# Kernel tuning notes

Measured on AMD Instinct MI355X. Metric: run time of the kernel, lower is better.

The kernel has to match this reference:

```python
import jax, jax.numpy as jnp
import numpy as np

B, T, D, H = 8, 4096, 128, 64


def setup_inputs() -> dict:
    key = jax.random.key(0)
    kx, kf, kg = jax.random.split(key, 3)
    X = jax.random.normal(kx, (B, T, D), dtype=jnp.float32)
    Wf = jax.random.normal(kf, (D, H), dtype=jnp.float32) * 0.05   # Conv1D k=1 weight
    Wg = jax.random.normal(kg, (3, D, H), dtype=jnp.float32) * 0.05  # Conv1D k=3 weight
    return {"X": X, "Wf": Wf, "Wg": Wg}


def reference(X, Wf, Wg):
    # f(X): pointwise conv == matmul over feature dim
    f = jnp.einsum('btd,dh->bth', X, Wf)
    # g(X): kernel-3 'same' conv, taps at offsets -1,0,+1
    Xp = jnp.pad(X, ((0, 0), (1, 1), (0, 0)))
    Tlen = X.shape[1]
    g = (jnp.einsum('btd,dh->bth', Xp[:, 0:Tlen], Wg[0])
         + jnp.einsum('btd,dh->bth', Xp[:, 1:Tlen + 1], Wg[1])
         + jnp.einsum('btd,dh->bth', Xp[:, 2:Tlen + 2], Wg[2]))
    # scores [B,T,T], scaled by sqrt(h)
    M = jnp.einsum('bth,bsh->bts', f, g) / jnp.sqrt(jnp.float32(H))
    w = jax.nn.softmax(M, axis=-1)
    # values are the raw input X
    return jnp.einsum('bts,bsd->btd', w, X)
```

## Files before the change

### kernel.cpp

```cpp
#include <hip/hip_runtime.h>
#include <hip/hip_bf16.h>

#define B_ 8
#define T_ 4096
#define D_ 128
#define H_ 64
#define SBLK 64
#define NT (T_ / SBLK)
#define NT2 (NT / 2)

typedef short bf16x8 __attribute__((ext_vector_type(8)));
typedef float f32x4 __attribute__((ext_vector_type(4)));
typedef float f32x16 __attribute__((ext_vector_type(16)));

__device__ __forceinline__ unsigned short f2bf(float f) {
  unsigned int u = __float_as_uint(f);
  u += 0x7fffu + ((u >> 16) & 1u);
  return (unsigned short)(u >> 16);
}

__device__ __forceinline__ void async_copy16(const void* g, void* l) {
  __builtin_amdgcn_global_load_lds((const __attribute__((address_space(1))) void*)g,
                                   (__attribute__((address_space(3))) void*)l, 16, 0, 0);
}

#define OFF_XP  0u
#define SZ_XP   ((unsigned)(B_*(T_+2)*D_*2))
#define OFF_XT  (OFF_XP + SZ_XP)
#define SZ_XT   ((unsigned)(B_*D_*T_*2))
#define OFF_F   (OFF_XT + SZ_XT)
#define SZ_F    ((unsigned)(B_*T_*H_*2))
#define OFF_G   (OFF_F + SZ_F)
#define OFF_WFT (OFF_G + SZ_F)
#define SZ_WFT  ((unsigned)(H_*D_*2))
#define OFF_WGT (OFF_WFT + SZ_WFT)
#define SZ_WGT  ((unsigned)(3*H_*D_*2))
#define OFF_PO1 (OFF_WGT + SZ_WGT)
#define SZ_PO1  ((unsigned)(B_*2048*D_*4))
#define OFF_PL  (OFF_PO1 + SZ_PO1)

#define SLOT(r) (((((r) & 3) << 1) ^ (((r) >> 2) & 1) ^ (((((r) >> 3) ^ ((r) >> 4)) & 1) << 2)))

__global__ __launch_bounds__(256) void prep_x(const float* __restrict__ X,
                                              unsigned short* __restrict__ Xp,
                                              unsigned short* __restrict__ XT) {
  __shared__ unsigned short tile[64][129];
  const int b = blockIdx.x;
  const int t0 = blockIdx.y * 64;
  const int tid = threadIdx.x;
#pragma unroll
  for (int c = 0; c < 8; ++c) {
    int i4 = tid + c * 256;
    int row = i4 >> 5, col4 = i4 & 31;
    float4 v = ((const float4*)X)[(size_t)(b * T_ + t0 + row) * 32 + col4];
    ushort4 h;
    h.x = f2bf(v.x); h.y = f2bf(v.y); h.z = f2bf(v.z); h.w = f2bf(v.w);
    ((ushort4*)Xp)[(size_t)(b * (T_ + 2) + 1 + t0 + row) * 32 + col4] = h;
    tile[row][col4 * 4 + 0] = h.x;
    tile[row][col4 * 4 + 1] = h.y;
    tile[row][col4 * 4 + 2] = h.z;
    tile[row][col4 * 4 + 3] = h.w;
  }
  if (blockIdx.y == 0 && tid < 32) {
    ushort4 z = {0, 0, 0, 0};
    ((ushort4*)Xp)[(size_t)(b * (T_ + 2) + 0) * 32 + tid] = z;
    ((ushort4*)Xp)[(size_t)(b * (T_ + 2) + T_ + 1) * 32 + tid] = z;
  }
  __syncthreads();
#pragma unroll
  for (int c = 0; c < 8; ++c) {
    int o4 = tid + c * 256;
    int d = o4 >> 4, t4 = o4 & 15;
    ushort4 h;
    h.x = tile[t4 * 4 + 0][d];
    h.y = tile[t4 * 4 + 1][d];
    h.z = tile[t4 * 4 + 2][d];
    h.w = tile[t4 * 4 + 3][d];
    ((ushort4*)XT)[(size_t)(b * 128 + d) * (T_ / 4) + (t0 >> 2) + t4] = h;
  }
}

__global__ __launch_bounds__(256) void prep_w(const float* __restrict__ Wf,
                                              const float* __restrict__ Wg,
                                              unsigned short* __restrict__ WfT,
                                              unsigned short* __restrict__ WgT) {
  const float SC = 0.18033688011112042f;
  int idx = blockIdx.x * 256 + threadIdx.x;
  if (idx < H_ * D_) {
    int h = idx >> 7, d = idx & 127;
    WfT[idx] = f2bf(Wf[d * H_ + h] * SC);
  } else {
    int j = idx - H_ * D_;
    int tap = j >> 13, r = j & 8191;
    int h = r >> 7, d = r & 127;
    WgT[j] = f2bf(Wg[tap * (D_ * H_) + d * H_ + h]);
  }
}

__global__ __launch_bounds__(64) void fg_kernel(const unsigned short* __restrict__ Xp,
                                                const unsigned short* __restrict__ WfT,
                                                const unsigned short* __restrict__ WgT,
                                                unsigned short* __restrict__ F,
                                                unsigned short* __restrict__ G) {
  const int lane = threadIdx.x;
  const int rowbase = blockIdx.x * 32;
  const int b = rowbase >> 12, t0 = rowbase & (T_ - 1);
  const int l15 = lane & 15, lhi = lane >> 4;
  const f32x4 fz = {0.f, 0.f, 0.f, 0.f};
  f32x4 accF[2][4], accG[2][4];
#pragma unroll
  for (int mt = 0; mt < 2; ++mt)
#pragma unroll
    for (int nt = 0; nt < 4; ++nt) { accF[mt][nt] = fz; accG[mt][nt] = fz; }

#pragma unroll
  for (int kk = 0; kk < 4; ++kk) {
    const int k0 = kk * 32 + lhi * 8;
    bf16x8 a[3][2];
#pragma unroll
    for (int sh = 0; sh < 3; ++sh)
#pragma unroll
      for (int mt = 0; mt < 2; ++mt) {
        int r = b * (T_ + 2) + t0 + sh + mt * 16 + l15;
        a[sh][mt] = *(const bf16x8*)&Xp[(size_t)r * 128 + k0];
      }
#pragma unroll
    for (int nt = 0; nt < 4; ++nt) {
      int h = nt * 16 + l15;
      bf16x8 wf  = *(const bf16x8*)&WfT[h * 128 + k0];
      bf16x8 wg0 = *(const bf16x8*)&WgT[(0 * 64 + h) * 128 + k0];
      bf16x8 wg1 = *(const bf16x8*)&WgT[(1 * 64 + h) * 128 + k0];
      bf16x8 wg2 = *(const bf16x8*)&WgT[(2 * 64 + h) * 128 + k0];
#pragma unroll
      for (int mt = 0; mt < 2; ++mt) {
        accF[mt][nt] = __builtin_amdgcn_mfma_f32_16x16x32_bf16(a[1][mt], wf,  accF[mt][nt], 0, 0, 0);
        accG[mt][nt] = __builtin_amdgcn_mfma_f32_16x16x32_bf16(a[0][mt], wg0, accG[mt][nt], 0, 0, 0);
        accG[mt][nt] = __builtin_amdgcn_mfma_f32_16x16x32_bf16(a[1][mt], wg1, accG[mt][nt], 0, 0, 0);
        accG[mt][nt] = __builtin_amdgcn_mfma_f32_16x16x32_bf16(a[2][mt], wg2, accG[mt][nt], 0, 0, 0);
      }
    }
  }
#pragma unroll
  for (int mt = 0; mt < 2; ++mt)
#pragma unroll
    for (int nt = 0; nt < 4; ++nt)
#pragma unroll
      for (int r = 0; r < 4; ++r) {
        int t = t0 + mt * 16 + lhi * 4 + r;
        int h = nt * 16 + l15;
        size_t o = (size_t)(b * T_ + t) * 64 + h;
        F[o] = f2bf(accF[mt][nt][r]);
        G[o] = f2bf(accG[mt][nt][r]);
      }
}

__global__ __launch_bounds__(256) void attn_kernel(const unsigned short* __restrict__ F,
                                                   const unsigned short* __restrict__ G,
                                                   const unsigned short* __restrict__ XT,
                                                   float* __restrict__ out,
                                                   float* __restrict__ PO0,
                                                   float* __restrict__ PO1,
                                                   float* __restrict__ PL) {
  __shared__ unsigned short klds[2][64 * 64];
  __shared__ unsigned short vlds[2][128 * 64];
  const int b = blockIdx.x;
  const int q0 = blockIdx.y * 128;
  const int z = blockIdx.z;
  const int tid = threadIdx.x;
  const int wave = tid >> 6, lane = tid & 63;
  const int l31 = lane & 31, hi = lane >> 5;
  const int qw = q0 + wave * 32;
  const int E = SLOT(l31) << 4;

  bf16x8 qf[4];
#pragma unroll
  for (int ks = 0; ks < 4; ++ks)
    qf[ks] = *(const bf16x8*)&F[(size_t)(b * T_ + qw + l31) * 64 + ks * 16 + hi * 8];

  f32x16 o_acc[4];
  f32x16 sacc;
#pragma unroll
  for (int r = 0; r < 16; ++r) sacc[r] = 0.f;
#pragma unroll
  for (int nt = 0; nt < 4; ++nt)
#pragma unroll
    for (int r = 0; r < 16; ++r) o_acc[nt][r] = 0.f;
  bf16x8 ones;
#pragma unroll
  for (int j = 0; j < 8; ++j) ones[j] = (short)0x3F80;

  const int lo3 = lane >> 3, lc = lane & 7;

  auto stage = [&](int buf, int s0n) {
#pragma unroll
    for (int i = 0; i < 2; ++i) {
      int kchunk = wave * 2 + i;
      int s = kchunk * 8 + lo3;
      int cp = lc ^ ((lo3 & 3) << 1) ^ ((lo3 >> 2) & 1) ^ (((kchunk ^ (kchunk >> 1)) & 1) << 2);
      async_copy16(&G[(size_t)(b * T_ + s0n + s) * 64 + cp * 8],
                   (char*)&klds[buf][0] + kchunk * 1024);
    }
#pragma unroll
    for (int i = 0; i < 4; ++i) {
      int vchunk = wave * 4 + i;
      int d = vchunk * 8 + lo3;
      int cp = lc ^ ((lo3 & 3) << 1) ^ ((lo3 >> 2) & 1) ^ (((vchunk ^ (vchunk >> 1)) & 1) << 2);
      async_copy16(&XT[(size_t)(b * 128 + d) * T_ + s0n + cp * 8],
                   (char*)&vlds[buf][0] + vchunk * 1024);
    }
  };

  stage(0, z * NT2 * SBLK);
  __syncthreads();

  union PW { unsigned u[4]; bf16x8 v; };

  for (int tt = 0; tt < NT2; ++tt) {
    const int cur = tt & 1;
    if (tt + 1 < NT2) stage(cur ^ 1, (z * NT2 + tt + 1) * SBLK);
    __builtin_amdgcn_s_setprio(1);

    char* kbase = (char*)klds[cur];
    char* vbase = (char*)vlds[cur];

    f32x16 S0, S1;
#pragma unroll
    for (int r = 0; r < 16; ++r) { S0[r] = 0.f; S1[r] = 0.f; }
#pragma unroll
    for (int ks = 0; ks < 4; ++ks) {
      bf16x8 k0 = *(const bf16x8*)(kbase + ((0 * 32 + l31) * 128 + ((ks * 32 + hi * 16) ^ E)));
      bf16x8 k1 = *(const bf16x8*)(kbase + ((1 * 32 + l31) * 128 + ((ks * 32 + hi * 16) ^ E)));
      S0 = __builtin_amdgcn_mfma_f32_32x32x16_bf16(k0, qf[ks], S0, 0, 0, 0);
      S1 = __builtin_amdgcn_mfma_f32_32x32x16_bf16(k1, qf[ks], S1, 0, 0, 0);
    }

    bf16x8 pa[4];
#pragma unroll
    for (int st = 0; st < 2; ++st) {
      const f32x16& S = st ? S1 : S0;
      float p[16];
#pragma unroll
      for (int r = 0; r < 16; ++r) p[r] = __builtin_amdgcn_exp2f(S[r]);
      unsigned w[4][2];
#pragma unroll
      for (int g = 0; g < 4; ++g)
#pragma unroll
        for (int u = 0; u < 2; ++u) {
          union { __hip_bfloat162 h2; unsigned uu; } cv;
          cv.h2 = __float22bfloat162_rn(make_float2(p[4 * g + 2 * u], p[4 * g + 2 * u + 1]));
          w[g][u] = cv.uu;
        }
#pragma unroll
      for (int ksl = 0; ksl < 2; ++ksl) {
        PW pw;
#pragma unroll
        for (int u = 0; u < 2; ++u) {
          unsigned A = w[2 * ksl][u], Bv = w[2 * ksl + 1][u];
          asm("v_permlane32_swap_b32 %0, %1" : "+v"(A), "+v"(Bv));
          pw.u[u] = A;
          pw.u[2 + u] = Bv;
        }
        pa[st * 2 + ksl] = pw.v;
      }
    }

#pragma unroll
    for (int ks = 0; ks < 4; ++ks)
      sacc = __builtin_amdgcn_mfma_f32_32x32x16_bf16(pa[ks], ones, sacc, 0, 0, 0);

#pragma unroll
    for (int nt = 0; nt < 4; ++nt) {
#pragma unroll
      for (int ks = 0; ks < 4; ++ks) {
        bf16x8 vf = *(const bf16x8*)(vbase + ((nt * 32 + l31) * 128 + ((ks * 32 + hi * 16) ^ E)));
        o_acc[nt] = __builtin_amdgcn_mfma_f32_32x32x16_bf16(pa[ks], vf, o_acc[nt], 0, 0, 0);
      }
    }
    __builtin_amdgcn_s_setprio(0);
    __syncthreads();
  }

  if (z == 1) {
#pragma unroll
    for (int r = 0; r < 16; ++r) {
      int trow = qw + (r & 3) + 8 * (r >> 2) + 4 * hi;
#pragma unroll
      for (int nt = 0; nt < 4; ++nt)
        out[(size_t)(b * T_ + trow) * 128 + nt * 32 + l31] = o_acc[nt][r];
    }
  } else {
    float* po = (q0 < 2048) ? PO0 : PO1;
#pragma unroll
    for (int r = 0; r < 16; ++r) {
      int trow = qw + (r & 3) + 8 * (r >> 2) + 4 * hi;
#pragma unroll
      for (int nt = 0; nt < 4; ++nt)
        po[(size_t)(b * 2048 + (trow & 2047)) * 128 + nt * 32 + l31] = o_acc[nt][r];
    }
  }
  if (l31 == 0) {
#pragma unroll
    for (int r = 0; r < 16; ++r) {
      int trow = qw + (r & 3) + 8 * (r >> 2) + 4 * hi;
      PL[z * (B_ * T_) + b * T_ + trow] = sacc[r];
    }
  }
}

__global__ __launch_bounds__(256) void merge_kernel(const float* __restrict__ PO0,
                                                    const float* __restrict__ PO1,
                                                    const float* __restrict__ PL,
                                                    float* __restrict__ out) {
  int idx = blockIdx.x * 256 + threadIdx.x;
  int row = idx >> 5;
  int b = row >> 12, t = row & (T_ - 1);
  const float4* po = (t < 2048) ? (const float4*)PO0 : (const float4*)PO1;
  float4 o = ((const float4*)out)[idx];
  float4 p = po[(size_t)(b * 2048 + (t & 2047)) * 32 + (idx & 31)];
  float inv = 1.0f / (PL[row] + PL[B_ * T_ + row]);
  float4 r;
  r.x = (o.x + p.x) * inv;
  r.y = (o.y + p.y) * inv;
  r.z = (o.z + p.z) * inv;
  r.w = (o.w + p.w) * inv;
  ((float4*)out)[idx] = r;
}

extern "C" void kernel_launch(void* const* d_in, const int* in_sizes, int n_in,
                              void* d_out, int out_size, void* d_ws, size_t ws_size,
                              hipStream_t stream) {
  (void)in_sizes; (void)n_in; (void)out_size; (void)ws_size;
  const float* X  = (const float*)d_in[0];
  const float* Wf = (const float*)d_in[1];
  const float* Wg = (const float*)d_in[2];
  float* out = (float*)d_out;
  char* ws = (char*)d_ws;
  unsigned short* Xp  = (unsigned short*)(ws + OFF_XP);
  unsigned short* XT  = (unsigned short*)(ws + OFF_XT);
  unsigned short* Fb  = (unsigned short*)(ws + OFF_F);
  unsigned short* Gb  = (unsigned short*)(ws + OFF_G);
  unsigned short* WfT = (unsigned short*)(ws + OFF_WFT);
  unsigned short* WgT = (unsigned short*)(ws + OFF_WGT);
  float* PO0 = (float*)(ws + OFF_XP);
  float* PO1 = (float*)(ws + OFF_PO1);
  float* PL  = (float*)(ws + OFF_PL);

  prep_x<<<dim3(B_, T_ / 64), 256, 0, stream>>>(X, Xp, XT);
  prep_w<<<(H_ * D_ * 4) / 256, 256, 0, stream>>>(Wf, Wg, WfT, WgT);
  fg_kernel<<<(B_ * T_) / 32, 64, 0, stream>>>(Xp, WfT, WgT, Fb, Gb);
  attn_kernel<<<dim3(B_, T_ / 128, 2), 256, 0, stream>>>(Fb, Gb, XT, out, PO0, PO1, PL);
  merge_kernel<<<(B_ * T_ * D_ / 4) / 256, 256, 0, stream>>>(PO0, PO1, PL, out);
}
```

Before: 100.9 us.

## Triple-buffer attention K/V staging with vmcnt waits; halve fg rows per block

The attention kernel moves from double to triple-buffered LDS staging of K (G) and V (XT) tiles, prefetching two tiles ahead. It waits with a partial s_waitcnt vmcnt plus a single barrier per iteration instead of a full __syncthreads after compute, so global-to-LDS copies can overlap more compute. Separately, the fg_kernel processes 16 rows per block instead of 32, doubling the grid for more parallelism at the cost of reloading weights more often. Triple buffering raises LDS use, and near the end of the loop it redundantly reloads the last tile to keep the vmcnt accounting consistent.

```diff
diff --git a/kernel.cpp b/kernel.cpp
--- a/kernel.cpp
+++ b/kernel.cpp
@@ -103,27 +103,23 @@
                                                 unsigned short* __restrict__ F,
                                                 unsigned short* __restrict__ G) {
   const int lane = threadIdx.x;
-  const int rowbase = blockIdx.x * 32;
+  const int rowbase = blockIdx.x * 16;
   const int b = rowbase >> 12, t0 = rowbase & (T_ - 1);
   const int l15 = lane & 15, lhi = lane >> 4;
   const f32x4 fz = {0.f, 0.f, 0.f, 0.f};
-  f32x4 accF[2][4], accG[2][4];
-#pragma unroll
-  for (int mt = 0; mt < 2; ++mt)
-#pragma unroll
-    for (int nt = 0; nt < 4; ++nt) { accF[mt][nt] = fz; accG[mt][nt] = fz; }
+  f32x4 accF[4], accG[4];
+#pragma unroll
+  for (int nt = 0; nt < 4; ++nt) { accF[nt] = fz; accG[nt] = fz; }
 
 #pragma unroll
   for (int kk = 0; kk < 4; ++kk) {
     const int k0 = kk * 32 + lhi * 8;
-    bf16x8 a[3][2];
-#pragma unroll
-    for (int sh = 0; sh < 3; ++sh)
-#pragma unroll
-      for (int mt = 0; mt < 2; ++mt) {
-        int r = b * (T_ + 2) + t0 + sh + mt * 16 + l15;
-        a[sh][mt] = *(const bf16x8*)&Xp[(size_t)r * 128 + k0];
-      }
+    bf16x8 a[3];
+#pragma unroll
+    for (int sh = 0; sh < 3; ++sh) {
+      int r = b * (T_ + 2) + t0 + sh + l15;
+      a[sh] = *(const bf16x8*)&Xp[(size_t)r * 128 + k0];
+    }
 #pragma unroll
     for (int nt = 0; nt < 4; ++nt) {
       int h = nt * 16 + l15;
@@ -131,27 +127,22 @@
       bf16x8 wg0 = *(const bf16x8*)&WgT[(0 * 64 + h) * 128 + k0];
       bf16x8 wg1 = *(const bf16x8*)&WgT[(1 * 64 + h) * 128 + k0];
       bf16x8 wg2 = *(const bf16x8*)&WgT[(2 * 64 + h) * 128 + k0];
-#pragma unroll
-      for (int mt = 0; mt < 2; ++mt) {
-        accF[mt][nt] = __builtin_amdgcn_mfma_f32_16x16x32_bf16(a[1][mt], wf,  accF[mt][nt], 0, 0, 0);
-        accG[mt][nt] = __builtin_amdgcn_mfma_f32_16x16x32_bf16(a[0][mt], wg0, accG[mt][nt], 0, 0, 0);
-        accG[mt][nt] = __builtin_amdgcn_mfma_f32_16x16x32_bf16(a[1][mt], wg1, accG[mt][nt], 0, 0, 0);
-        accG[mt][nt] = __builtin_amdgcn_mfma_f32_16x16x32_bf16(a[2][mt], wg2, accG[mt][nt], 0, 0, 0);
-      }
-    }
-  }
-#pragma unroll
-  for (int mt = 0; mt < 2; ++mt)
-#pragma unroll
-    for (int nt = 0; nt < 4; ++nt)
-#pragma unroll
-      for (int r = 0; r < 4; ++r) {
-        int t = t0 + mt * 16 + lhi * 4 + r;
-        int h = nt * 16 + l15;
-        size_t o = (size_t)(b * T_ + t) * 64 + h;
-        F[o] = f2bf(accF[mt][nt][r]);
-        G[o] = f2bf(accG[mt][nt][r]);
-      }
+      accF[nt] = __builtin_amdgcn_mfma_f32_16x16x32_bf16(a[1], wf,  accF[nt], 0, 0, 0);
+      accG[nt] = __builtin_amdgcn_mfma_f32_16x16x32_bf16(a[0], wg0, accG[nt], 0, 0, 0);
+      accG[nt] = __builtin_amdgcn_mfma_f32_16x16x32_bf16(a[1], wg1, accG[nt], 0, 0, 0);
+      accG[nt] = __builtin_amdgcn_mfma_f32_16x16x32_bf16(a[2], wg2, accG[nt], 0, 0, 0);
+    }
+  }
+#pragma unroll
+  for (int nt = 0; nt < 4; ++nt)
+#pragma unroll
+    for (int r = 0; r < 4; ++r) {
+      int t = t0 + lhi * 4 + r;
+      int h = nt * 16 + l15;
+      size_t o = (size_t)(b * T_ + t) * 64 + h;
+      F[o] = f2bf(accF[nt][r]);
+      G[o] = f2bf(accG[nt][r]);
+    }
 }
 
 __global__ __launch_bounds__(256) void attn_kernel(const unsigned short* __restrict__ F,
@@ -161,8 +152,8 @@
                                                    float* __restrict__ PO0,
                                                    float* __restrict__ PO1,
                                                    float* __restrict__ PL) {
-  __shared__ unsigned short klds[2][64 * 64];
-  __shared__ unsigned short vlds[2][128 * 64];
+  __shared__ unsigned short klds[3][64 * 64];
+  __shared__ unsigned short vlds[3][128 * 64];
   const int b = blockIdx.x;
   const int q0 = blockIdx.y * 128;
   const int z = blockIdx.z;
@@ -191,14 +182,15 @@
 
   const int lo3 = lane >> 3, lc = lane & 7;
 
-  auto stage = [&](int buf, int s0n) {
+  auto stage = [&](unsigned short* kdst, unsigned short* vdst, int gt) {
+    const int s0n = gt * SBLK;
 #pragma unroll
     for (int i = 0; i < 2; ++i) {
       int kchunk = wave * 2 + i;
       int s = kchunk * 8 + lo3;
       int cp = lc ^ ((lo3 & 3) << 1) ^ ((lo3 >> 2) & 1) ^ (((kchunk ^ (kchunk >> 1)) & 1) << 2);
       async_copy16(&G[(size_t)(b * T_ + s0n + s) * 64 + cp * 8],
-                   (char*)&klds[buf][0] + kchunk * 1024);
+                   (char*)kdst + kchunk * 1024);
     }
 #pragma unroll
     for (int i = 0; i < 4; ++i) {
@@ -206,22 +198,29 @@
       int d = vchunk * 8 + lo3;
       int cp = lc ^ ((lo3 & 3) << 1) ^ ((lo3 >> 2) & 1) ^ (((vchunk ^ (vchunk >> 1)) & 1) << 2);
       async_copy16(&XT[(size_t)(b * 128 + d) * T_ + s0n + cp * 8],
-                   (char*)&vlds[buf][0] + vchunk * 1024);
+                   (char*)vdst + vchunk * 1024);
     }
   };
 
-  stage(0, z * NT2 * SBLK);
-  __syncthreads();
+  stage(klds[0], vlds[0], z * NT2 + 0);
+  stage(klds[1], vlds[1], z * NT2 + 1);
+  unsigned short *kc = klds[0], *k1p = klds[1], *k2p = klds[2];
+  unsigned short *vc = vlds[0], *v1p = vlds[1], *v2p = vlds[2];
 
   union PW { unsigned u[4]; bf16x8 v; };
 
   for (int tt = 0; tt < NT2; ++tt) {
-    const int cur = tt & 1;
-    if (tt + 1 < NT2) stage(cur ^ 1, (z * NT2 + tt + 1) * SBLK);
+    asm volatile("s_waitcnt vmcnt(6)" ::: "memory");
+    __builtin_amdgcn_sched_barrier(0);
+    __builtin_amdgcn_s_barrier();
+    __builtin_amdgcn_sched_barrier(0);
+
+    int nxt = tt + 2; if (nxt > NT2 - 1) nxt = NT2 - 1;
+    stage(k2p, v2p, z * NT2 + nxt);
+
+    char* kbase = (char*)kc;
+    char* vbase = (char*)vc;
     __builtin_amdgcn_s_setprio(1);
-
-    char* kbase = (char*)klds[cur];
-    char* vbase = (char*)vlds[cur];
 
     f32x16 S0, S1;
 #pragma unroll
@@ -277,7 +276,9 @@
       }
     }
     __builtin_amdgcn_s_setprio(0);
-    __syncthreads();
+
+    unsigned short* tk = kc; kc = k1p; k1p = k2p; k2p = tk;
+    unsigned short* tv = vc; vc = v1p; v1p = v2p; v2p = tv;
   }
 
   if (z == 1) {
@@ -347,7 +348,7 @@
 
   prep_x<<<dim3(B_, T_ / 64), 256, 0, stream>>>(X, Xp, XT);
   prep_w<<<(H_ * D_ * 4) / 256, 256, 0, stream>>>(Wf, Wg, WfT, WgT);
-  fg_kernel<<<(B_ * T_) / 32, 64, 0, stream>>>(Xp, WfT, WgT, Fb, Gb);
+  fg_kernel<<<(B_ * T_) / 16, 64, 0, stream>>>(Xp, WfT, WgT, Fb, Gb);
   attn_kernel<<<dim3(B_, T_ / 128, 2), 256, 0, stream>>>(Fb, Gb, XT, out, PO0, PO1, PL);
   merge_kernel<<<(B_ * T_ * D_ / 4) / 256, 256, 0, stream>>>(PO0, PO1, PL, out);
 }
```

Result: slower. 107.5 us (+6.6%).

## Split attention keys three ways with fp16 partials and scalar row-sum

Applied to the files above, without the earlier changes.

Raises the key-dimension split from two to three (22/21/21 tiles), so the grid has 768 blocks instead of 512 and spreads better across CUs. Partial outputs are stored in fp16 instead of fp32 to cut merge traffic. The row sum is now a VALU reduction of the exponentials plus one shuffle, replacing the MFMA against a ones vector. The trade-off is an extra partial buffer and fp16 rounding of unnormalized partial outputs, which could overflow or lose precision.

```diff
diff --git a/kernel.cpp b/kernel.cpp
--- a/kernel.cpp
+++ b/kernel.cpp
@@ -7,11 +7,11 @@
 #define H_ 64
 #define SBLK 64
 #define NT (T_ / SBLK)
-#define NT2 (NT / 2)
 
 typedef short bf16x8 __attribute__((ext_vector_type(8)));
 typedef float f32x4 __attribute__((ext_vector_type(4)));
 typedef float f32x16 __attribute__((ext_vector_type(16)));
+typedef _Float16 h4 __attribute__((ext_vector_type(4)));
 
 __device__ __forceinline__ unsigned short f2bf(float f) {
   unsigned int u = __float_as_uint(f);
@@ -35,9 +35,9 @@
 #define SZ_WFT  ((unsigned)(H_*D_*2))
 #define OFF_WGT (OFF_WFT + SZ_WFT)
 #define SZ_WGT  ((unsigned)(3*H_*D_*2))
-#define OFF_PO1 (OFF_WGT + SZ_WGT)
-#define SZ_PO1  ((unsigned)(B_*2048*D_*4))
-#define OFF_PL  (OFF_PO1 + SZ_PO1)
+#define OFF_PH1 (OFF_WGT + SZ_WGT)
+#define SZ_PH1  ((unsigned)(B_*T_*D_*2))
+#define OFF_PL  (OFF_PH1 + SZ_PH1)
 
 #define SLOT(r) (((((r) & 3) << 1) ^ (((r) >> 2) & 1) ^ (((((r) >> 3) ^ ((r) >> 4)) & 1) << 2)))
 
@@ -158,14 +158,16 @@
                                                    const unsigned short* __restrict__ G,
                                                    const unsigned short* __restrict__ XT,
                                                    float* __restrict__ out,
-                                                   float* __restrict__ PO0,
-                                                   float* __restrict__ PO1,
+                                                   _Float16* __restrict__ PH0,
+                                                   _Float16* __restrict__ PH1,
                                                    float* __restrict__ PL) {
   __shared__ unsigned short klds[2][64 * 64];
   __shared__ unsigned short vlds[2][128 * 64];
   const int b = blockIdx.x;
   const int q0 = blockIdx.y * 128;
   const int z = blockIdx.z;
+  const int t_begin = (z == 0) ? 0 : 22 + (z - 1) * 21;
+  const int t_count = (z == 0) ? 22 : 21;
   const int tid = threadIdx.x;
   const int wave = tid >> 6, lane = tid & 63;
   const int l31 = lane & 31, hi = lane >> 5;
@@ -178,20 +180,16 @@
     qf[ks] = *(const bf16x8*)&F[(size_t)(b * T_ + qw + l31) * 64 + ks * 16 + hi * 8];
 
   f32x16 o_acc[4];
-  f32x16 sacc;
-#pragma unroll
-  for (int r = 0; r < 16; ++r) sacc[r] = 0.f;
 #pragma unroll
   for (int nt = 0; nt < 4; ++nt)
 #pragma unroll
     for (int r = 0; r < 16; ++r) o_acc[nt][r] = 0.f;
-  bf16x8 ones;
-#pragma unroll
-  for (int j = 0; j < 8; ++j) ones[j] = (short)0x3F80;
+  float lsum = 0.f;
 
   const int lo3 = lane >> 3, lc = lane & 7;
 
-  auto stage = [&](int buf, int s0n) {
+  auto stage = [&](int buf, int gt) {
+    const int s0n = gt * SBLK;
 #pragma unroll
     for (int i = 0; i < 2; ++i) {
       int kchunk = wave * 2 + i;
@@ -210,14 +208,14 @@
     }
   };
 
-  stage(0, z * NT2 * SBLK);
+  stage(0, t_begin);
   __syncthreads();
 
   union PW { unsigned u[4]; bf16x8 v; };
 
-  for (int tt = 0; tt < NT2; ++tt) {
+  for (int tt = 0; tt < t_count; ++tt) {
     const int cur = tt & 1;
-    if (tt + 1 < NT2) stage(cur ^ 1, (z * NT2 + tt + 1) * SBLK);
+    if (tt + 1 < t_count) stage(cur ^ 1, t_begin + tt + 1);
     __builtin_amdgcn_s_setprio(1);
 
     char* kbase = (char*)klds[cur];
@@ -241,6 +239,8 @@
       float p[16];
 #pragma unroll
       for (int r = 0; r < 16; ++r) p[r] = __builtin_amdgcn_exp2f(S[r]);
+      lsum += (((p[0] + p[1]) + (p[2] + p[3])) + ((p[4] + p[5]) + (p[6] + p[7])))
+            + (((p[8] + p[9]) + (p[10] + p[11])) + ((p[12] + p[13]) + (p[14] + p[15])));
       unsigned w[4][2];
 #pragma unroll
       for (int g = 0; g < 4; ++g)
@@ -265,10 +265,6 @@
     }
 
 #pragma unroll
-    for (int ks = 0; ks < 4; ++ks)
-      sacc = __builtin_amdgcn_mfma_f32_32x32x16_bf16(pa[ks], ones, sacc, 0, 0, 0);
-
-#pragma unroll
     for (int nt = 0; nt < 4; ++nt) {
 #pragma unroll
       for (int ks = 0; ks < 4; ++ks) {
@@ -280,7 +276,7 @@
     __syncthreads();
   }
 
-  if (z == 1) {
+  if (z == 2) {
 #pragma unroll
     for (int r = 0; r < 16; ++r) {
       int trow = qw + (r & 3) + 8 * (r >> 2) + 4 * hi;
@@ -289,40 +285,35 @@
         out[(size_t)(b * T_ + trow) * 128 + nt * 32 + l31] = o_acc[nt][r];
     }
   } else {
-    float* po = (q0 < 2048) ? PO0 : PO1;
+    _Float16* ph = z ? PH1 : PH0;
 #pragma unroll
     for (int r = 0; r < 16; ++r) {
       int trow = qw + (r & 3) + 8 * (r >> 2) + 4 * hi;
 #pragma unroll
       for (int nt = 0; nt < 4; ++nt)
-        po[(size_t)(b * 2048 + (trow & 2047)) * 128 + nt * 32 + l31] = o_acc[nt][r];
-    }
-  }
-  if (l31 == 0) {
-#pragma unroll
-    for (int r = 0; r < 16; ++r) {
-      int trow = qw + (r & 3) + 8 * (r >> 2) + 4 * hi;
-      PL[z * (B_ * T_) + b * T_ + trow] = sacc[r];
-    }
-  }
-}
-
-__global__ __launch_bounds__(256) void merge_kernel(const float* __restrict__ PO0,
-                                                    const float* __restrict__ PO1,
+        ph[(size_t)(b * T_ + trow) * 128 + nt * 32 + l31] = (_Float16)o_acc[nt][r];
+    }
+  }
+  lsum += __shfl_xor(lsum, 32, 64);
+  if (hi == 0)
+    PL[z * (B_ * T_) + b * T_ + qw + l31] = lsum;
+}
+
+__global__ __launch_bounds__(256) void merge_kernel(const _Float16* __restrict__ PH0,
+                                                    const _Float16* __restrict__ PH1,
                                                     const float* __restrict__ PL,
                                                     float* __restrict__ out) {
   int idx = blockIdx.x * 256 + threadIdx.x;
   int row = idx >> 5;
-  int b = row >> 12, t = row & (T_ - 1);
-  const float4* po = (t < 2048) ? (const float4*)PO0 : (const float4*)PO1;
   float4 o = ((const float4*)out)[idx];
-  float4 p = po[(size_t)(b * 2048 + (t & 2047)) * 32 + (idx & 31)];
-  float inv = 1.0f / (PL[row] + PL[B_ * T_ + row]);
+  h4 p0 = *(const h4*)&PH0[(size_t)idx * 4];
+  h4 p1 = *(const h4*)&PH1[(size_t)idx * 4];
+  float inv = 1.0f / (PL[row] + PL[B_ * T_ + row] + PL[2 * B_ * T_ + row]);
   float4 r;
-  r.x = (o.x + p.x) * inv;
-  r.y = (o.y + p.y) * inv;
-  r.z = (o.z + p.z) * inv;
-  r.w = (o.w + p.w) * inv;
+  r.x = (o.x + (float)p0.x + (float)p1.x) * inv;
+  r.y = (o.y + (float)p0.y + (float)p1.y) * inv;
+  r.z = (o.z + (float)p0.z + (float)p1.z) * inv;
+  r.w = (o.w + (float)p0.w + (float)p1.w) * inv;
   ((float4*)out)[idx] = r;
 }
 
@@ -341,13 +332,13 @@
   unsigned short* Gb  = (unsigned short*)(ws + OFF_G);
   unsigned short* WfT = (unsigned short*)(ws + OFF_WFT);
   unsigned short* WgT = (unsigned short*)(ws + OFF_WGT);
-  float* PO0 = (float*)(ws + OFF_XP);
-  float* PO1 = (float*)(ws + OFF_PO1);
+  _Float16* PH0 = (_Float16*)(ws + OFF_XP);
+  _Float16* PH1 = (_Float16*)(ws + OFF_PH1);
   float* PL  = (float*)(ws + OFF_PL);
 
   prep_x<<<dim3(B_, T_ / 64), 256, 0, stream>>>(X, Xp, XT);
   prep_w<<<(H_ * D_ * 4) / 256, 256, 0, stream>>>(Wf, Wg, WfT, WgT);
   fg_kernel<<<(B_ * T_) / 32, 64, 0, stream>>>(Xp, WfT, WgT, Fb, Gb);
-  attn_kernel<<<dim3(B_, T_ / 128, 2), 256, 0, stream>>>(Fb, Gb, XT, out, PO0, PO1, PL);
-  merge_kernel<<<(B_ * T_ * D_ / 4) / 256, 256, 0, stream>>>(PO0, PO1, PL, out);
-}
+  attn_kernel<<<dim3(B_, T_ / 128, 3), 256, 0, stream>>>(Fb, Gb, XT, out, PH0, PH1, PL);
+  merge_kernel<<<(B_ * T_ * D_ / 4) / 256, 256, 0, stream>>>(PH0, PH1, PL, out);
+}
```

Result: slower. 114.8 us (+13.8%).
